# Kernel tuning notes

Measured on AMD Instinct MI355X. Metric: run time of the kernel, lower is better.

Reference implementation:

```python
import jax, jax.numpy as jnp
import numpy as np
from jax import lax

D = 32          # link_state_dim == path_state_dim
MAX_LEN = 16    # max path length (fixed for jit)
T_ITER = 8      # message-passing iterations


def gru_cell(x, h, kernel, rec_kernel, bias):
    """Keras GRUCell, reset_after=True. bias: [2, 3H] (input bias, recurrent bias)."""
    xw = x @ kernel + bias[0]
    hw = h @ rec_kernel + bias[1]
    xz, xr, xh = jnp.split(xw, 3, axis=-1)
    hz, hr, hh = jnp.split(hw, 3, axis=-1)
    z = jax.nn.sigmoid(xz + hz)
    r = jax.nn.sigmoid(xr + hr)
    c = jnp.tanh(xh + r * hh)
    return z * h + (1.0 - z) * c


def setup_inputs() -> dict:
    n_paths, n_links = 100000, 10000
    lengths = (np.arange(n_paths) % MAX_LEN) + 1            # 1..16, avg 8.5
    E = int(lengths.sum())                                   # 850000
    path_ids = np.repeat(np.arange(n_paths), lengths).astype(np.int32)
    offsets = np.repeat(np.cumsum(lengths) - lengths, lengths)
    sequence_path = (np.arange(E) - offsets).astype(np.int32)  # 0..len-1 per path
    rng = np.random.default_rng(0)
    link_to_path = rng.integers(0, n_links, E).astype(np.int32)

    key = jax.random.key(0)
    ks = jax.random.split(key, 16)
    p = {
        'capacity': jax.random.uniform(ks[0], (n_links, 1), jnp.float32) + 0.1,
        'traffic': jax.random.uniform(ks[1], (n_paths, 1), jnp.float32),
        'packets': jax.random.uniform(ks[2], (n_paths, 1), jnp.float32),
        'time_dist_params': jax.random.normal(ks[3], (n_paths, 12), jnp.float32),
        'path_kernel': 0.2 * jax.random.normal(ks[4], (D, 3 * D), jnp.float32),
        'path_rec_kernel': 0.2 * jax.random.normal(ks[5], (D, 3 * D), jnp.float32),
        'path_bias': jnp.zeros((2, 3 * D), jnp.float32),
        'link_kernel': 0.2 * jax.random.normal(ks[6], (D, 3 * D), jnp.float32),
        'link_rec_kernel': 0.2 * jax.random.normal(ks[7], (D, 3 * D), jnp.float32),
        'link_bias': jnp.zeros((2, 3 * D), jnp.float32),
        'w1': 0.1 * jax.random.normal(ks[8], (D, 256), jnp.float32),
        'b1': jnp.zeros((256,), jnp.float32),
        'w2': 0.1 * jax.random.normal(ks[9], (256, 256), jnp.float32),
        'b2': jnp.zeros((256,), jnp.float32),
        'w3': 0.1 * jax.random.normal(ks[10], (256, 1), jnp.float32),
        'b3': jnp.zeros((1,), jnp.float32),
        'link_to_path': jnp.asarray(link_to_path),
        'path_ids': jnp.asarray(path_ids),
        'sequence_path': jnp.asarray(sequence_path),
        'path_to_link': jnp.asarray(path_ids),      # path index of each (link,path) incidence
        'sequence_links': jnp.asarray(link_to_path),  # link index (segment id) of each incidence
        'n_links': n_links,
        'n_paths': n_paths,
    }
    return p


def reference(capacity, traffic, packets, time_dist_params,
              path_kernel, path_rec_kernel, path_bias,
              link_kernel, link_rec_kernel, link_bias,
              w1, b1, w2, b2, w3, b3,
              link_to_path, path_ids, sequence_path, path_to_link, sequence_links,
              n_links, n_paths):
    # initial states
    link_state = jnp.concatenate([capacity, jnp.zeros((n_links, D - 1), capacity.dtype)], axis=1)
    path_state = jnp.concatenate(
        [traffic, packets, time_dist_params, jnp.zeros((n_paths, D - 14), traffic.dtype)], axis=1)

    def mp_iter(carry, _):
        link_state, path_state = carry
        # gather link states along each path, scatter into padded [P, T, D]
        link_gather = link_state[link_to_path]
        link_inputs = jnp.zeros((n_paths, MAX_LEN, D), link_state.dtype)
        link_inputs = link_inputs.at[path_ids, sequence_path].set(link_gather)
        xs = jnp.moveaxis(link_inputs, 1, 0)              # [T, P, D]
        mask = jnp.any(xs != 0.0, axis=-1)                # keras Masking semantics

        def rnn_step(h, xm):
            x, m = xm
            h_new = gru_cell(x, h, path_kernel, path_rec_kernel, path_bias)
            return jnp.where(m[:, None], h_new, h), None

        path_state, _ = lax.scan(rnn_step, path_state, (xs, mask))
        # aggregate path states back onto links
        path_gather = path_state[path_to_link]
        path_sum = jax.ops.segment_sum(path_gather, sequence_links, num_segments=n_links)
        link_state = gru_cell(path_sum, link_state, link_kernel, link_rec_kernel, link_bias)
        return (link_state, path_state), None

    (link_state, path_state), _ = lax.scan(mp_iter, (link_state, path_state), None, length=T_ITER)

    h = jax.nn.relu(path_state @ w1 + b1)
    h = jax.nn.relu(h @ w2 + b2)
    return h @ w3 + b3
```

## Files before the change

kernel.cpp:

```cpp
#include <hip/hip_runtime.h>
#include <hip/hip_bf16.h>

#define DD 32
#define GG 96

typedef __attribute__((ext_vector_type(8))) short bf16x8;
typedef __attribute__((ext_vector_type(4))) float f32x4;

__device__ __forceinline__ float frcp(float x){ return __builtin_amdgcn_rcpf(x); }
__device__ __forceinline__ float fsig(float x){
    float e = __expf(-x);
    return frcp(1.0f + e);
}
__device__ __forceinline__ float ftanh(float x){
    float ax = fabsf(x);
    float e  = __expf(-2.0f * ax);
    float t  = (1.0f - e) * frcp(1.0f + e);
    return copysignf(t, x);
}
__device__ __forceinline__ short f2bf(float f){
    union { float f; unsigned u; } v; v.f = f;
    unsigned r = v.u + 0x7fffu + ((v.u >> 16) & 1u);
    return (short)(r >> 16);
}
__device__ __forceinline__ float bf2f(short s){
    union { unsigned u; float f; } v; v.u = ((unsigned)(unsigned short)s) << 16;
    return v.f;
}
__device__ __forceinline__ void split2(float x, short& hi, short& lo){
    hi = f2bf(x);
    lo = f2bf(x - bf2f(hi));
}
__device__ __forceinline__ f32x4 splat4(float x){ f32x4 v = { x, x, x, x }; return v; }

#define MFMA3(acc, ah, al, bh, bl) do { \
    acc = __builtin_amdgcn_mfma_f32_16x16x32_bf16(ah, bh, acc, 0, 0, 0); \
    acc = __builtin_amdgcn_mfma_f32_16x16x32_bf16(al, bh, acc, 0, 0, 0); \
    acc = __builtin_amdgcn_mfma_f32_16x16x32_bf16(ah, bl, acc, 0, 0, 0); \
} while (0)


__global__ void zero_ints_kernel(int* a, int n){
    int i = blockIdx.x * blockDim.x + threadIdx.x;
    if (i < n) a[i] = 0;
}

__global__ void init_states_kernel(const float* __restrict__ cap,
                                   const float* __restrict__ traffic, const float* __restrict__ packets,
                                   const float* __restrict__ tdp,
                                   float* __restrict__ ls, short* __restrict__ lsbh, short* __restrict__ lsbl,
                                   float* __restrict__ ps, int n_links, int n_paths){
    int i = blockIdx.x * blockDim.x + threadIdx.x;
    int nl = n_links * DD;
    if (i < nl){
        int l = i >> 5, d = i & 31;
        float v = (d == 0) ? cap[l] : 0.0f;
        ls[i] = v;
        short hi, lo; split2(v, hi, lo);
        lsbh[i] = hi; lsbl[i] = lo;
        return;
    }
    int j = i - nl;
    if (j >= n_paths * DD) return;
    int p = j >> 5, d = j & 31;
    float v = 0.0f;
    if (d == 0) v = traffic[p];
    else if (d == 1) v = packets[p];
    else if (d < 14) v = tdp[p * 12 + (d - 2)];
    ps[j] = v;
}

__global__ void meta_kernel(const int* __restrict__ path_ids, const int* __restrict__ seqp,
                            const int* __restrict__ seql, int* __restrict__ start,
                            int* __restrict__ lenp, int* __restrict__ lcount, int E){
    int e = blockIdx.x * blockDim.x + threadIdx.x;
    if (e >= E) return;
    int p = path_ids[e];
    int s = seqp[e];
    if (s == 0) start[p] = e;
    if (e == E - 1 || path_ids[e + 1] != p) lenp[p] = s + 1;
    atomicAdd(&lcount[seql[e]], 1);
}

__global__ void bhist_block_kernel(const int* __restrict__ lenp, int* __restrict__ bcnt,
                                   int* __restrict__ bh, int n_paths){
    __shared__ int h[16];
    if (threadIdx.x < 16) h[threadIdx.x] = 0;
    __syncthreads();
    int p = blockIdx.x * 256 + threadIdx.x;
    if (p < n_paths) atomicAdd(&h[lenp[p] - 1], 1);
    __syncthreads();
    if (threadIdx.x < 16){
        bh[blockIdx.x * 16 + threadIdx.x] = h[threadIdx.x];
        atomicAdd(&bcnt[threadIdx.x], h[threadIdx.x]);
    }
}

__global__ void bscan2_kernel(const int* __restrict__ bcnt, const int* __restrict__ bh,
                              int* __restrict__ bb, int nblk){
    __shared__ int base[16];
    if (threadIdx.x == 0){
        int run = 0;
        for (int i = 0; i < 16; i++){ base[i] = run; run += bcnt[i]; }
    }
    __syncthreads();
    int i = threadIdx.x;
    if (i < 16){
        int run = base[i];
        for (int blk = 0; blk < nblk; ++blk){
            bb[blk * 16 + i] = run;
            run += bh[blk * 16 + i];
        }
    }
}

__global__ void bscatter2_kernel(const int* __restrict__ lenp, const int* __restrict__ bb,
                                 int* __restrict__ order, int n_paths){
    __shared__ int h[16];
    if (threadIdx.x < 16) h[threadIdx.x] = 0;
    __syncthreads();
    int p = blockIdx.x * 256 + threadIdx.x;
    if (p < n_paths){
        int b = lenp[p] - 1;
        int r = atomicAdd(&h[b], 1);
        order[bb[blockIdx.x * 16 + b] + r] = p;
    }
}

__global__ __launch_bounds__(1024) void scan_kernel(const int* __restrict__ cnt, int* __restrict__ off, int n){
    __shared__ int psh[1025];
    int tid = threadIdx.x;
    int chunk = (n + 1023) / 1024;
    int b = tid * chunk, e = min(b + chunk, n);
    int s = 0;
    for (int i = b; i < e; ++i) s += cnt[i];
    psh[tid + 1] = s;
    if (tid == 0) psh[0] = 0;
    __syncthreads();
    for (int ofs = 1; ofs < 1024; ofs <<= 1){
        int v = (tid + 1 >= ofs) ? psh[tid + 1 - ofs] : 0;
        __syncthreads();
        psh[tid + 1] += v;
        __syncthreads();
    }
    int run = psh[tid];
    for (int i = b; i < e; ++i){ off[i] = run; run += cnt[i]; }
    if (b < n && e == n) off[n] = run;
}

__global__ void fillpbl_kernel(const int* __restrict__ seql, const int* __restrict__ p2l,
                               const int* __restrict__ loff, int* __restrict__ lfill,
                               int* __restrict__ pbl, int E){
    int e = blockIdx.x * blockDim.x + threadIdx.x;
    if (e >= E) return;
    int l = seql[e];
    int pos = loff[l] + atomicAdd(&lfill[l], 1);
    pbl[pos] = p2l[e];
}

__global__ void pack_all_kernel(const float* __restrict__ pK, const float* __restrict__ pRK,
                                const float* __restrict__ lK, const float* __restrict__ lRK,
                                const float* __restrict__ w1, const float* __restrict__ w2,
                                short* __restrict__ gth, short* __restrict__ gtl,
                                short* __restrict__ rth, short* __restrict__ rtl){
    int t0 = blockIdx.x * blockDim.x + threadIdx.x;
    if (t0 < 4 * 6 * 64){
        int t = t0;
        int lane = t & 63;
        int jt = (t >> 6) % 6;
        int mat = t / (6 * 64);
        const float* W = (mat == 0) ? pK : (mat == 1) ? pRK : (mat == 2) ? lK : lRK;
        int n = lane & 15, g = lane >> 4;
        for (int i = 0; i < 8; i++){
            float w = W[(g * 8 + i) * GG + jt * 16 + n];
            short hi, lo; split2(w, hi, lo);
            gth[(size_t)t * 8 + i] = hi;
            gtl[(size_t)t * 8 + i] = lo;
        }
        return;
    }
    int t = t0 - 4 * 6 * 64;
    if (t >= 144 * 64) return;
    int lane = t & 63;
    int f = t >> 6;
    int n = lane & 15, g = lane >> 4;
    for (int i = 0; i < 8; i++){
        float w;
        if (f < 16) w = w1[(g * 8 + i) * 256 + f * 16 + n];
        else {
            int ff = f - 16, kc = ff >> 4, jt = ff & 15;
            w = w2[(kc * 32 + g * 8 + i) * 256 + jt * 16 + n];
        }
        short hi, lo; split2(w, hi, lo);
        rth[(size_t)t * 8 + i] = hi;
        rtl[(size_t)t * 8 + i] = lo;
    }
}


template<bool MASK>
__device__ __forceinline__ void gru_gates(const f32x4 accZR[4], const f32x4 accXC[2], const f32x4 accHC[2],
                                          float hD[2][4], int la, int t)
{
    #pragma unroll
    for (int tt = 0; tt < 2; tt++){
        #pragma unroll
        for (int r = 0; r < 4; r++){
            float z = fsig(accZR[tt][r]);
            float rr = fsig(accZR[2 + tt][r]);
            float c = ftanh(accXC[tt][r] + rr * accHC[tt][r]);
            float hn = z * hD[tt][r] + (1.0f - z) * c;
            if (MASK) hD[tt][r] = (t < la) ? hn : hD[tt][r];
            else      hD[tt][r] = hn;
        }
    }
}

__device__ __forceinline__ void hD_to_bfrag(const float hD[2][4], int l15, int g,
                                            bf16x8& bh, bf16x8& bl){
    unsigned pk0[4], pk1[4];
    #pragma unroll
    for (int r = 0; r < 4; r++){
        short hi, lo;
        split2(hD[0][r], hi, lo);
        pk0[r] = (((unsigned)(unsigned short)hi) << 16) | (unsigned)(unsigned short)lo;
        split2(hD[1][r], hi, lo);
        pk1[r] = (((unsigned)(unsigned short)hi) << 16) | (unsigned)(unsigned short)lo;
    }
    bool hiTT = ((g >> 1) & 1);
    #pragma unroll
    for (int i = 0; i < 8; i++){
        int src = l15 + 16 * ((2 * g + (i >> 2)) & 3);
        unsigned v0 = (unsigned)__shfl((int)pk0[i & 3], src, 64);
        unsigned v1 = (unsigned)__shfl((int)pk1[i & 3], src, 64);
        unsigned v = hiTT ? v1 : v0;
        bh[i] = (short)(v >> 16);
        bl[i] = (short)(v & 0xffffu);
    }
}

__device__ __forceinline__ void load_bias4(const float* __restrict__ bias, int g,
                                           f32x4 bZR[4], f32x4 bXC[2], f32x4 bHC[2]){
    #pragma unroll
    for (int jt = 0; jt < 4; jt++)
        #pragma unroll
        for (int r = 0; r < 4; r++)
            bZR[jt][r] = bias[jt * 16 + 4 * g + r] + bias[GG + jt * 16 + 4 * g + r];
    #pragma unroll
    for (int u = 0; u < 2; u++)
        #pragma unroll
        for (int r = 0; r < 4; r++){
            bXC[u][r] = bias[(4 + u) * 16 + 4 * g + r];
            bHC[u][r] = bias[GG + (4 + u) * 16 + 4 * g + r];
        }
}

__global__ __launch_bounds__(256, 1) void path_gru_kernel(
    const short* __restrict__ lsbh, const short* __restrict__ lsbl, float* __restrict__ ps,
    const int* __restrict__ l2p, const int* __restrict__ start,
    const int* __restrict__ lenp, const int* __restrict__ order,
    const short* __restrict__ gth, const short* __restrict__ gtl,
    const float* __restrict__ bias, int n_paths, int n_waves, int stride)
{
    int tid = threadIdx.x;
    int warp = tid >> 6;
    int lane = tid & 63;
    int l15 = lane & 15, g = lane >> 4;

    int gw = blockIdx.x * 4 + warp;
    int nw = gridDim.x * 4;

    bf16x8 wKh[6], wKl[6], wRKh[6], wRKl[6];
    #pragma unroll
    for (int jt = 0; jt < 6; jt++){
        wKh[jt]  = *(const bf16x8*)(gth + ((size_t)((0 * 6 + jt) * 64 + lane)) * 8);
        wKl[jt]  = *(const bf16x8*)(gtl + ((size_t)((0 * 6 + jt) * 64 + lane)) * 8);
        wRKh[jt] = *(const bf16x8*)(gth + ((size_t)((1 * 6 + jt) * 64 + lane)) * 8);
        wRKl[jt] = *(const bf16x8*)(gtl + ((size_t)((1 * 6 + jt) * 64 + lane)) * 8);
    }
    f32x4 bZR[4], bXC[2], bHC[2];
    load_bias4(bias, g, bZR, bXC, bHC);

    for (int w = gw; w < n_waves; w += nw){
        long long wp = ((long long)w * stride) % n_waves;
        int base16 = (int)wp * 16;

        int aidx = base16 + l15;
        bool va = (aidx < n_paths);
        int pa = order[min(aidx, n_paths - 1)];
        int s0 = start[pa];
        int la_c = lenp[pa];
        int la = va ? la_c : 0;
        int maxlen = __shfl(la_c, 15);

        float hD[2][4];
        {
            float4 h0 = *(const float4*)(ps + (size_t)pa * DD + 4 * g);
            float4 h1 = *(const float4*)(ps + (size_t)pa * DD + 16 + 4 * g);
            hD[0][0] = h0.x; hD[0][1] = h0.y; hD[0][2] = h0.z; hD[0][3] = h0.w;
            hD[1][0] = h1.x; hD[1][1] = h1.y; hD[1][2] = h1.z; hD[1][3] = h1.w;
        }

        bf16x8 hfh, hfl;
        hD_to_bfrag(hD, l15, g, hfh, hfl);

        bf16x8 xfh, xfl;
        {
            int lk = l2p[s0];
            xfh = *reinterpret_cast<const bf16x8*>(lsbh + (size_t)lk * DD + g * 8);
            xfl = *reinterpret_cast<const bf16x8*>(lsbl + (size_t)lk * DD + g * 8);
        }

        for (int t = 0; t < maxlen; ++t){
            bf16x8 nxh, nxl;
            int tn = t + 1;
            if (tn < maxlen){
                int e = s0 + max(min(tn, la - 1), 0);
                int lk = l2p[e];
                nxh = *reinterpret_cast<const bf16x8*>(lsbh + (size_t)lk * DD + g * 8);
                nxl = *reinterpret_cast<const bf16x8*>(lsbl + (size_t)lk * DD + g * 8);
            }

            f32x4 accZR[4], accXC[2], accHC[2];
            #pragma unroll
            for (int jt = 0; jt < 4; jt++){
                f32x4 a = bZR[jt];
                MFMA3(a, wKh[jt],  wKl[jt],  xfh, xfl);
                MFMA3(a, wRKh[jt], wRKl[jt], hfh, hfl);
                accZR[jt] = a;
            }
            #pragma unroll
            for (int u = 0; u < 2; u++){
                f32x4 ax = bXC[u];
                MFMA3(ax, wKh[4 + u], wKl[4 + u], xfh, xfl);
                accXC[u] = ax;
                f32x4 ah = bHC[u];
                MFMA3(ah, wRKh[4 + u], wRKl[4 + u], hfh, hfl);
                accHC[u] = ah;
            }

            gru_gates<true>(accZR, accXC, accHC, hD, la, t);
            hD_to_bfrag(hD, l15, g, hfh, hfl);

            xfh = nxh; xfl = nxl;
        }

        if (va){
            float4 h0 = { hD[0][0], hD[0][1], hD[0][2], hD[0][3] };
            float4 h1 = { hD[1][0], hD[1][1], hD[1][2], hD[1][3] };
            *(float4*)(ps + (size_t)pa * DD + 4 * g) = h0;
            *(float4*)(ps + (size_t)pa * DD + 16 + 4 * g) = h1;
        }
    }
}

__global__ __launch_bounds__(256, 1) void link_fused_kernel(
    const float* __restrict__ ps, const int* __restrict__ loff, const int* __restrict__ pbl,
    float* __restrict__ ls, short* __restrict__ lsbh, short* __restrict__ lsbl,
    const short* __restrict__ gth, const short* __restrict__ gtl,
    const float* __restrict__ bias, int n_links)
{
    int tid = threadIdx.x;
    int warp = tid >> 6;
    int lane = tid & 63;
    int l15 = lane & 15, g = lane >> 4;

    int base16 = (blockIdx.x * 4 + warp) * 16;
    if (base16 >= n_links) return;

    bf16x8 wKh[6], wKl[6], wRKh[6], wRKl[6];
    #pragma unroll
    for (int jt = 0; jt < 6; jt++){
        wKh[jt]  = *(const bf16x8*)(gth + ((size_t)((2 * 6 + jt) * 64 + lane)) * 8);
        wKl[jt]  = *(const bf16x8*)(gtl + ((size_t)((2 * 6 + jt) * 64 + lane)) * 8);
        wRKh[jt] = *(const bf16x8*)(gth + ((size_t)((3 * 6 + jt) * 64 + lane)) * 8);
        wRKl[jt] = *(const bf16x8*)(gtl + ((size_t)((3 * 6 + jt) * 64 + lane)) * 8);
    }
    f32x4 bZR[4], bXC[2], bHC[2];
    load_bias4(bias, g, bZR, bXC, bHC);

    int di = base16 + l15;
    bool va = (di < n_links);
    int pa = min(di, n_links - 1);

    float4 s0v = {0,0,0,0}, s1v = {0,0,0,0};
    {
        int b = loff[pa], e = loff[pa + 1];
        #pragma unroll 4
        for (int k = b; k < e; ++k){
            const float4* pr = (const float4*)(ps + (size_t)pbl[k] * DD) + g * 2;
            float4 v0 = pr[0], v1 = pr[1];
            s0v.x += v0.x; s0v.y += v0.y; s0v.z += v0.z; s0v.w += v0.w;
            s1v.x += v1.x; s1v.y += v1.y; s1v.z += v1.z; s1v.w += v1.w;
        }
    }

    float hD[2][4];
    {
        float4 h0 = *(const float4*)(ls + (size_t)pa * DD + 4 * g);
        float4 h1 = *(const float4*)(ls + (size_t)pa * DD + 16 + 4 * g);
        hD[0][0] = h0.x; hD[0][1] = h0.y; hD[0][2] = h0.z; hD[0][3] = h0.w;
        hD[1][0] = h1.x; hD[1][1] = h1.y; hD[1][2] = h1.z; hD[1][3] = h1.w;
    }
    bf16x8 hfh = *reinterpret_cast<const bf16x8*>(lsbh + (size_t)pa * DD + g * 8);
    bf16x8 hfl = *reinterpret_cast<const bf16x8*>(lsbl + (size_t)pa * DD + g * 8);

    bf16x8 xfh, xfl;
    {
        float xs[8] = { s0v.x, s0v.y, s0v.z, s0v.w, s1v.x, s1v.y, s1v.z, s1v.w };
        #pragma unroll
        for (int i = 0; i < 8; i++){
            short hi, lo; split2(xs[i], hi, lo);
            xfh[i] = hi; xfl[i] = lo;
        }
    }

    f32x4 accZR[4], accXC[2], accHC[2];
    #pragma unroll
    for (int jt = 0; jt < 4; jt++){
        f32x4 a = bZR[jt];
        MFMA3(a, wKh[jt],  wKl[jt],  xfh, xfl);
        MFMA3(a, wRKh[jt], wRKl[jt], hfh, hfl);
        accZR[jt] = a;
    }
    #pragma unroll
    for (int u = 0; u < 2; u++){
        f32x4 ax = bXC[u];
        MFMA3(ax, wKh[4 + u], wKl[4 + u], xfh, xfl);
        accXC[u] = ax;
        f32x4 ah = bHC[u];
        MFMA3(ah, wRKh[4 + u], wRKl[4 + u], hfh, hfl);
        accHC[u] = ah;
    }
    gru_gates<false>(accZR, accXC, accHC, hD, 0, 0);

    if (va){
        float4 h0 = { hD[0][0], hD[0][1], hD[0][2], hD[0][3] };
        float4 h1 = { hD[1][0], hD[1][1], hD[1][2], hD[1][3] };
        *(float4*)(ls + (size_t)pa * DD + 4 * g) = h0;
        *(float4*)(ls + (size_t)pa * DD + 16 + 4 * g) = h1;
        short hs[8], lws[8];
        #pragma unroll
        for (int r = 0; r < 4; r++){ split2(hD[0][r], hs[r], lws[r]); split2(hD[1][r], hs[4 + r], lws[4 + r]); }
        *(short4*)(lsbh + (size_t)pa * DD + 4 * g)      = make_short4(hs[0], hs[1], hs[2], hs[3]);
        *(short4*)(lsbh + (size_t)pa * DD + 16 + 4 * g) = make_short4(hs[4], hs[5], hs[6], hs[7]);
        *(short4*)(lsbl + (size_t)pa * DD + 4 * g)      = make_short4(lws[0], lws[1], lws[2], lws[3]);
        *(short4*)(lsbl + (size_t)pa * DD + 16 + 4 * g) = make_short4(lws[4], lws[5], lws[6], lws[7]);
    }
}

__global__ __launch_bounds__(256) void readout_kernel(
    const float* __restrict__ ps,
    const short* __restrict__ rth, const short* __restrict__ rtl,
    const float* __restrict__ b1, const float* __restrict__ b2,
    const float* __restrict__ w3, const float* __restrict__ b3,
    float* __restrict__ out, int n_paths)
{
    __shared__ __align__(16) float hT[4][16 * 68];

    int tid = threadIdx.x;
    int warp = tid >> 6;
    int lane = tid & 63;
    int l15 = lane & 15, g = lane >> 4;
    int pbase = blockIdx.x * 64 + warp * 16;

    bf16x8 xh, xl;
    {
        int prow = min(pbase + l15, n_paths - 1);
        const float* xp = ps + (size_t)prow * DD + g * 8;
        #pragma unroll
        for (int i = 0; i < 8; i++){ short hi, lo; split2(xp[i], hi, lo); xh[i] = hi; xl[i] = lo; }
    }

    float* hw = hT[warp];

    f32x4 acc2[16];
    #pragma unroll
    for (int jt = 0; jt < 16; jt++) acc2[jt] = splat4(b2[jt * 16 + l15]);

    #pragma unroll 1
    for (int c = 0; c < 4; c++){
        #pragma unroll
        for (int u = 0; u < 4; u++){
            int jt = c * 4 + u;
            bf16x8 wh = *(const bf16x8*)(rth + (size_t)(jt * 64 + lane) * 8);
            bf16x8 wl = *(const bf16x8*)(rtl + (size_t)(jt * 64 + lane) * 8);
            f32x4 a = splat4(b1[jt * 16 + l15]);
            MFMA3(a, xh, xl, wh, wl);
            #pragma unroll
            for (int r = 0; r < 4; r++)
                hw[(g * 4 + r) * 68 + u * 16 + l15] = fmaxf(a[r], 0.0f);
        }
        bf16x8 ah[2], al[2];
        #pragma unroll
        for (int kc2 = 0; kc2 < 2; kc2++){
            const float* hr = hw + l15 * 68 + kc2 * 32 + g * 8;
            #pragma unroll
            for (int i = 0; i < 8; i++){ short hi, lo; split2(hr[i], hi, lo); ah[kc2][i] = hi; al[kc2][i] = lo; }
        }
        #pragma unroll
        for (int jt = 0; jt < 16; jt++){
            #pragma unroll
            for (int kc2 = 0; kc2 < 2; kc2++){
                int f = 16 + (c * 2 + kc2) * 16 + jt;
                bf16x8 wh = *(const bf16x8*)(rth + (size_t)(f * 64 + lane) * 8);
                bf16x8 wl = *(const bf16x8*)(rtl + (size_t)(f * 64 + lane) * 8);
                MFMA3(acc2[jt], ah[kc2], al[kc2], wh, wl);
            }
        }
    }

    float part[4] = {0.0f, 0.0f, 0.0f, 0.0f};
    #pragma unroll
    for (int jt = 0; jt < 16; jt++){
        float w3v = w3[jt * 16 + l15];
        #pragma unroll
        for (int r = 0; r < 4; r++)
            part[r] = fmaf(fmaxf(acc2[jt][r], 0.0f), w3v, part[r]);
    }
    #pragma unroll
    for (int ofs = 1; ofs < 16; ofs <<= 1)
        #pragma unroll
        for (int r = 0; r < 4; r++)
            part[r] += __shfl_xor(part[r], ofs);

    if (l15 == 0){
        float b3v = b3[0];
        #pragma unroll
        for (int r = 0; r < 4; r++){
            int p = pbase + g * 4 + r;
            if (p < n_paths) out[p] = part[r] + b3v;
        }
    }
}

static int host_gcd(int a, int b){ while (b){ int t = a % b; a = b; b = t; } return a; }

extern "C" void kernel_launch(void* const* d_in, const int* in_sizes, int n_in,
                              void* d_out, int out_size, void* d_ws, size_t ws_size,
                              hipStream_t stream)
{
    const float* capacity = (const float*)d_in[0];
    const float* traffic  = (const float*)d_in[1];
    const float* packets  = (const float*)d_in[2];
    const float* tdp      = (const float*)d_in[3];
    const float* pK  = (const float*)d_in[4];
    const float* pRK = (const float*)d_in[5];
    const float* pB  = (const float*)d_in[6];
    const float* lK  = (const float*)d_in[7];
    const float* lRK = (const float*)d_in[8];
    const float* lB  = (const float*)d_in[9];
    const float* w1  = (const float*)d_in[10];
    const float* b1  = (const float*)d_in[11];
    const float* w2  = (const float*)d_in[12];
    const float* b2  = (const float*)d_in[13];
    const float* w3  = (const float*)d_in[14];
    const float* b3  = (const float*)d_in[15];
    const int* l2p      = (const int*)d_in[16];
    const int* path_ids = (const int*)d_in[17];
    const int* seqp     = (const int*)d_in[18];
    const int* p2l      = (const int*)d_in[19];
    const int* seql     = (const int*)d_in[20];
    int n_links = in_sizes[0];
    int n_paths = in_sizes[1];
    int E       = in_sizes[16];
    float* out = (float*)d_out;

    char* w = (char*)d_ws;
    auto carve = [&](size_t bytes) -> void* {
        void* r = (void*)w;
        w += (bytes + 255) & ~(size_t)255;
        return r;
    };
    int nblk = (n_paths + 255) / 256;
    float* ls    = (float*)carve((size_t)n_links * DD * 4);
    short* lsbh  = (short*)carve((size_t)n_links * DD * 2);
    short* lsbl  = (short*)carve((size_t)n_links * DD * 2);
    float* ps    = (float*)carve((size_t)n_paths * DD * 4);
    int* start   = (int*)carve((size_t)n_paths * 4);
    int* lenp    = (int*)carve((size_t)n_paths * 4);
    int* order   = (int*)carve((size_t)n_paths * 4);
    int* loff    = (int*)carve((size_t)(n_links + 1) * 4);
    int* pbl     = (int*)carve((size_t)E * 4);
    short* gth   = (short*)carve((size_t)4 * 6 * 64 * 8 * 2);
    short* gtl   = (short*)carve((size_t)4 * 6 * 64 * 8 * 2);
    short* rth   = (short*)carve((size_t)144 * 64 * 8 * 2);
    short* rtl   = (short*)carve((size_t)144 * 64 * 8 * 2);
    int* bh      = (int*)carve((size_t)nblk * 16 * 4);
    int* bb      = (int*)carve((size_t)nblk * 16 * 4);
    int* izero   = (int*)carve(((size_t)2 * n_links + 16) * 4);
    int* lcount  = izero;
    int* lfill   = izero + n_links;
    int* bcnt    = izero + 2 * n_links;

    const int TB = 256;
    int nz = 2 * n_links + 16;
    zero_ints_kernel<<<(nz + TB - 1) / TB, TB, 0, stream>>>(izero, nz);
    init_states_kernel<<<(((n_links + n_paths) * DD) + TB - 1) / TB, TB, 0, stream>>>(
        capacity, traffic, packets, tdp, ls, lsbh, lsbl, ps, n_links, n_paths);
    meta_kernel<<<(E + TB - 1) / TB, TB, 0, stream>>>(path_ids, seqp, seql, start, lenp, lcount, E);
    bhist_block_kernel<<<nblk, 256, 0, stream>>>(lenp, bcnt, bh, n_paths);
    bscan2_kernel<<<1, 64, 0, stream>>>(bcnt, bh, bb, nblk);
    bscatter2_kernel<<<nblk, 256, 0, stream>>>(lenp, bb, order, n_paths);
    scan_kernel<<<1, 1024, 0, stream>>>(lcount, loff, n_links);
    fillpbl_kernel<<<(E + TB - 1) / TB, TB, 0, stream>>>(seql, p2l, loff, lfill, pbl, E);
    pack_all_kernel<<<((4 * 6 * 64 + 144 * 64) + TB - 1) / TB, TB, 0, stream>>>(
        pK, pRK, lK, lRK, w1, w2, gth, gtl, rth, rtl);

    int n_waves = (n_paths + 15) / 16;
    int stride = 1;
    if (n_waves > 2){
        stride = (int)((double)n_waves * 0.381966);
        if (stride < 1) stride = 1;
        while (host_gcd(stride, n_waves) != 1) stride++;
    }
    int pg_blocks = 512;
    if (pg_blocks > (n_waves + 3) / 4) pg_blocks = (n_waves + 3) / 4;
    int lg_blocks = ((n_links + 15) / 16 + 3) / 4;

    for (int it = 0; it < 8; ++it){
        path_gru_kernel<<<pg_blocks, 256, 0, stream>>>(lsbh, lsbl, ps, l2p, start, lenp, order,
                                                       gth, gtl, pB, n_paths, n_waves, stride);
        link_fused_kernel<<<lg_blocks, 256, 0, stream>>>(ps, loff, pbl, ls, lsbh, lsbl,
                                                         gth, gtl, lB, n_links);
    }
    readout_kernel<<<(n_paths + 63) / 64, 256, 0, stream>>>(ps, rth, rtl, b1, b2, w3, b3, out, n_paths);
}
```

Before: 1.188 ms.

## Interleave two path tiles per wave in path GRU and launch one wave per pair

Each wave now processes two adjacent length-sorted 16-path tiles together, interleaving their MFMA chains and gate math so the two independent recurrences hide each other's latency. The grid-stride loop with a golden-ratio permutation is replaced by a direct launch of one wave per tile pair, with no persistent cap on blocks. The next-step gather is now issued unconditionally each step. The cost is higher register pressure from two sets of state and fragments, and the loop runs to the longer of the two tiles' max lengths.

```diff
diff --git a/kernel.cpp b/kernel.cpp
--- a/kernel.cpp
+++ b/kernel.cpp
@@ -197,7 +197,6 @@
     }
 }
 
-
 template<bool MASK>
 __device__ __forceinline__ void gru_gates(const f32x4 accZR[4], const f32x4 accXC[2], const f32x4 accHC[2],
                                           float hD[2][4], int la, int t)
@@ -260,7 +259,7 @@
     const int* __restrict__ l2p, const int* __restrict__ start,
     const int* __restrict__ lenp, const int* __restrict__ order,
     const short* __restrict__ gth, const short* __restrict__ gtl,
-    const float* __restrict__ bias, int n_paths, int n_waves, int stride)
+    const float* __restrict__ bias, int n_paths, int n_waves, int n_pairs)
 {
     int tid = threadIdx.x;
     int warp = tid >> 6;
@@ -281,75 +280,120 @@
     f32x4 bZR[4], bXC[2], bHC[2];
     load_bias4(bias, g, bZR, bXC, bHC);
 
-    for (int w = gw; w < n_waves; w += nw){
-        long long wp = ((long long)w * stride) % n_waves;
-        int base16 = (int)wp * 16;
-
-        int aidx = base16 + l15;
-        bool va = (aidx < n_paths);
-        int pa = order[min(aidx, n_paths - 1)];
-        int s0 = start[pa];
-        int la_c = lenp[pa];
-        int la = va ? la_c : 0;
-        int maxlen = __shfl(la_c, 15);
-
-        float hD[2][4];
+    for (int p = gw; p < n_pairs; p += nw){
+        int cA = p * 2, cB = cA + 1;
+
+        int aidxA = cA * 16 + l15;
+        bool vA = (aidxA < n_paths);
+        int paA = order[min(aidxA, n_paths - 1)];
+        int s0A = start[paA];
+        int lacA = lenp[paA];
+        int laA = vA ? lacA : 0;
+        int mlA = __shfl(lacA, 15);
+
+        float hDA[2][4];
         {
-            float4 h0 = *(const float4*)(ps + (size_t)pa * DD + 4 * g);
-            float4 h1 = *(const float4*)(ps + (size_t)pa * DD + 16 + 4 * g);
-            hD[0][0] = h0.x; hD[0][1] = h0.y; hD[0][2] = h0.z; hD[0][3] = h0.w;
-            hD[1][0] = h1.x; hD[1][1] = h1.y; hD[1][2] = h1.z; hD[1][3] = h1.w;
-        }
-
-        bf16x8 hfh, hfl;
-        hD_to_bfrag(hD, l15, g, hfh, hfl);
-
-        bf16x8 xfh, xfl;
+            float4 h0 = *(const float4*)(ps + (size_t)paA * DD + 4 * g);
+            float4 h1 = *(const float4*)(ps + (size_t)paA * DD + 16 + 4 * g);
+            hDA[0][0] = h0.x; hDA[0][1] = h0.y; hDA[0][2] = h0.z; hDA[0][3] = h0.w;
+            hDA[1][0] = h1.x; hDA[1][1] = h1.y; hDA[1][2] = h1.z; hDA[1][3] = h1.w;
+        }
+        bf16x8 hfhA, hflA;
+        hD_to_bfrag(hDA, l15, g, hfhA, hflA);
+        bf16x8 xfhA = *reinterpret_cast<const bf16x8*>(lsbh + (size_t)l2p[s0A] * DD + g * 8);
+        bf16x8 xflA = *reinterpret_cast<const bf16x8*>(lsbl + (size_t)l2p[s0A] * DD + g * 8);
+
+        bool okB = (cB < n_waves);
+        int aidxB = min(cB, n_waves - 1) * 16 + l15;
+        bool vB = okB && (aidxB < n_paths);
+        int paB = order[min(aidxB, n_paths - 1)];
+        int s0B = start[paB];
+        int lacB = lenp[paB];
+        int laB = vB ? lacB : 0;
+        int mlB = okB ? __shfl(lacB, 15) : 0;
+
+        float hDB[2][4];
         {
-            int lk = l2p[s0];
-            xfh = *reinterpret_cast<const bf16x8*>(lsbh + (size_t)lk * DD + g * 8);
-            xfl = *reinterpret_cast<const bf16x8*>(lsbl + (size_t)lk * DD + g * 8);
-        }
-
-        for (int t = 0; t < maxlen; ++t){
-            bf16x8 nxh, nxl;
+            float4 h0 = *(const float4*)(ps + (size_t)paB * DD + 4 * g);
+            float4 h1 = *(const float4*)(ps + (size_t)paB * DD + 16 + 4 * g);
+            hDB[0][0] = h0.x; hDB[0][1] = h0.y; hDB[0][2] = h0.z; hDB[0][3] = h0.w;
+            hDB[1][0] = h1.x; hDB[1][1] = h1.y; hDB[1][2] = h1.z; hDB[1][3] = h1.w;
+        }
+        bf16x8 hfhB, hflB;
+        hD_to_bfrag(hDB, l15, g, hfhB, hflB);
+        bf16x8 xfhB = *reinterpret_cast<const bf16x8*>(lsbh + (size_t)l2p[s0B] * DD + g * 8);
+        bf16x8 xflB = *reinterpret_cast<const bf16x8*>(lsbl + (size_t)l2p[s0B] * DD + g * 8);
+
+        int T = max(mlA, mlB);
+        for (int t = 0; t < T; ++t){
             int tn = t + 1;
-            if (tn < maxlen){
-                int e = s0 + max(min(tn, la - 1), 0);
-                int lk = l2p[e];
-                nxh = *reinterpret_cast<const bf16x8*>(lsbh + (size_t)lk * DD + g * 8);
-                nxl = *reinterpret_cast<const bf16x8*>(lsbl + (size_t)lk * DD + g * 8);
+            int eA = s0A + max(min(tn, laA - 1), 0);
+            int eB = s0B + max(min(tn, laB - 1), 0);
+            int lkA = l2p[eA], lkB = l2p[eB];
+            bf16x8 nxhA = *reinterpret_cast<const bf16x8*>(lsbh + (size_t)lkA * DD + g * 8);
+            bf16x8 nxlA = *reinterpret_cast<const bf16x8*>(lsbl + (size_t)lkA * DD + g * 8);
+            bf16x8 nxhB = *reinterpret_cast<const bf16x8*>(lsbh + (size_t)lkB * DD + g * 8);
+            bf16x8 nxlB = *reinterpret_cast<const bf16x8*>(lsbl + (size_t)lkB * DD + g * 8);
+
+            {
+                f32x4 accZR[4], accXC[2], accHC[2];
+                #pragma unroll
+                for (int jt = 0; jt < 4; jt++){
+                    f32x4 a = bZR[jt];
+                    MFMA3(a, wKh[jt],  wKl[jt],  xfhA, xflA);
+                    MFMA3(a, wRKh[jt], wRKl[jt], hfhA, hflA);
+                    accZR[jt] = a;
+                }
+                #pragma unroll
+                for (int u = 0; u < 2; u++){
+                    f32x4 ax = bXC[u];
+                    MFMA3(ax, wKh[4 + u], wKl[4 + u], xfhA, xflA);
+                    accXC[u] = ax;
+                    f32x4 ah = bHC[u];
+                    MFMA3(ah, wRKh[4 + u], wRKl[4 + u], hfhA, hflA);
+                    accHC[u] = ah;
+                }
+                gru_gates<true>(accZR, accXC, accHC, hDA, laA, t);
+                hD_to_bfrag(hDA, l15, g, hfhA, hflA);
             }
 
-            f32x4 accZR[4], accXC[2], accHC[2];
-            #pragma unroll
-            for (int jt = 0; jt < 4; jt++){
-                f32x4 a = bZR[jt];
-                MFMA3(a, wKh[jt],  wKl[jt],  xfh, xfl);
-                MFMA3(a, wRKh[jt], wRKl[jt], hfh, hfl);
-                accZR[jt] = a;
+            {
+                f32x4 accZR[4], accXC[2], accHC[2];
+                #pragma unroll
+                for (int jt = 0; jt < 4; jt++){
+                    f32x4 a = bZR[jt];
+                    MFMA3(a, wKh[jt],  wKl[jt],  xfhB, xflB);
+                    MFMA3(a, wRKh[jt], wRKl[jt], hfhB, hflB);
+                    accZR[jt] = a;
+                }
+                #pragma unroll
+                for (int u = 0; u < 2; u++){
+                    f32x4 ax = bXC[u];
+                    MFMA3(ax, wKh[4 + u], wKl[4 + u], xfhB, xflB);
+                    accXC[u] = ax;
+                    f32x4 ah = bHC[u];
+                    MFMA3(ah, wRKh[4 + u], wRKl[4 + u], hfhB, hflB);
+                    accHC[u] = ah;
+                }
+                gru_gates<true>(accZR, accXC, accHC, hDB, laB, t);
+                hD_to_bfrag(hDB, l15, g, hfhB, hflB);
             }
-            #pragma unroll
-            for (int u = 0; u < 2; u++){
-                f32x4 ax = bXC[u];
-                MFMA3(ax, wKh[4 + u], wKl[4 + u], xfh, xfl);
-                accXC[u] = ax;
-                f32x4 ah = bHC[u];
-                MFMA3(ah, wRKh[4 + u], wRKl[4 + u], hfh, hfl);
-                accHC[u] = ah;
-            }
-
-            gru_gates<true>(accZR, accXC, accHC, hD, la, t);
-            hD_to_bfrag(hD, l15, g, hfh, hfl);
-
-            xfh = nxh; xfl = nxl;
-        }
-
-        if (va){
-            float4 h0 = { hD[0][0], hD[0][1], hD[0][2], hD[0][3] };
-            float4 h1 = { hD[1][0], hD[1][1], hD[1][2], hD[1][3] };
-            *(float4*)(ps + (size_t)pa * DD + 4 * g) = h0;
-            *(float4*)(ps + (size_t)pa * DD + 16 + 4 * g) = h1;
+
+            xfhA = nxhA; xflA = nxlA;
+            xfhB = nxhB; xflB = nxlB;
+        }
+
+        if (vA){
+            float4 h0 = { hDA[0][0], hDA[0][1], hDA[0][2], hDA[0][3] };
+            float4 h1 = { hDA[1][0], hDA[1][1], hDA[1][2], hDA[1][3] };
+            *(float4*)(ps + (size_t)paA * DD + 4 * g) = h0;
+            *(float4*)(ps + (size_t)paA * DD + 16 + 4 * g) = h1;
+        }
+        if (vB){
+            float4 h0 = { hDB[0][0], hDB[0][1], hDB[0][2], hDB[0][3] };
+            float4 h1 = { hDB[1][0], hDB[1][1], hDB[1][2], hDB[1][3] };
+            *(float4*)(ps + (size_t)paB * DD + 4 * g) = h0;
+            *(float4*)(ps + (size_t)paB * DD + 16 + 4 * g) = h1;
         }
     }
 }
@@ -533,8 +577,6 @@
         }
     }
 }
-
-static int host_gcd(int a, int b){ while (b){ int t = a % b; a = b; b = t; } return a; }
 
 extern "C" void kernel_launch(void* const* d_in, const int* in_sizes, int n_in,
                               void* d_out, int out_size, void* d_ws, size_t ws_size,
@@ -608,19 +650,13 @@
         pK, pRK, lK, lRK, w1, w2, gth, gtl, rth, rtl);
 
     int n_waves = (n_paths + 15) / 16;
-    int stride = 1;
-    if (n_waves > 2){
-        stride = (int)((double)n_waves * 0.381966);
-        if (stride < 1) stride = 1;
-        while (host_gcd(stride, n_waves) != 1) stride++;
-    }
-    int pg_blocks = 512;
-    if (pg_blocks > (n_waves + 3) / 4) pg_blocks = (n_waves + 3) / 4;
+    int n_pairs = (n_waves + 1) / 2;
+    int pg_blocks = (n_pairs + 3) / 4;
     int lg_blocks = ((n_links + 15) / 16 + 3) / 4;
 
     for (int it = 0; it < 8; ++it){
         path_gru_kernel<<<pg_blocks, 256, 0, stream>>>(lsbh, lsbl, ps, l2p, start, lenp, order,
-                                                       gth, gtl, pB, n_paths, n_waves, stride);
+                                                       gth, gtl, pB, n_paths, n_waves, n_pairs);
         link_fused_kernel<<<lg_blocks, 256, 0, stream>>>(ps, loff, pbl, ls, lsbh, lsbl,
                                                          gth, gtl, lB, n_links);
     }
```

Result: slower. 1.274 ms (+7.2%).
